# Performance work log

Hardware: AMD Instinct MI355X
Metric: run time of the kernel (lower is better)

Reference implementation:

```python
import jax, jax.numpy as jnp
import numpy as np

SMOOTHNESS_WEIGHT = 0.01
TRANSITION_PENALTY_WEIGHT = 0.1
NUM_CLASSES = 3

B, C, T = 512, 3, 16384


def setup_inputs() -> dict:
    key = jax.random.key(0)
    k1, k2 = jax.random.split(key)
    logits = jax.random.normal(k1, (B, C, T), dtype=jnp.float32)
    labels = jax.random.randint(k2, (B, T), 0, NUM_CLASSES, dtype=jnp.int64)
    return {"logits": logits, "labels": labels}


def reference(logits, labels):
    # --- cross entropy (mean over all B*T positions), logits [B, C, T] ---
    logp = jax.nn.log_softmax(logits, axis=1)                      # [B, C, T]
    nll = -jnp.take_along_axis(logp, labels[:, None, :], axis=1)   # [B, 1, T]
    ce = jnp.mean(nll)

    # --- smoothness: mean squared temporal difference of logits ---
    diff = jnp.mean((logits[:, :, 1:] - logits[:, :, :-1]) ** 2)
    smoothness_penalty = SMOOTHNESS_WEIGHT * diff

    # --- transition penalty: mean penalty over invalid (prev, next) pairs ---
    preds = jnp.argmax(logits, axis=1)                             # [B, T]
    # penalty lookup table: invalid transitions (0->2), (2->1), (1->0) = 1
    table = (jnp.zeros((NUM_CLASSES, NUM_CLASSES), dtype=jnp.float32)
             .at[0, 2].set(1.0).at[2, 1].set(1.0).at[1, 0].set(1.0))
    vals = table[preds[:, :-1], preds[:, 1:]]                      # [B, T-1]
    count = jnp.sum(vals > 0)
    # mean over invalid transitions only; 0.0 if none occur
    transition_penalty = TRANSITION_PENALTY_WEIGHT * jnp.where(
        count > 0, jnp.sum(vals) / jnp.maximum(count, 1).astype(vals.dtype), 0.0)

    return ce + smoothness_penalty + transition_penalty
```

## Files before the change

kernel.cpp:

```cpp
#include <hip/hip_runtime.h>

typedef float v4f __attribute__((ext_vector_type(4)));
typedef int   v4i __attribute__((ext_vector_type(4)));

#define BB 512
#define CC 3
#define TT 16384
#define NBLK 2048
#define NTHREADS (NBLK * 256)
#define NQUAD (BB * TT / 4)
#define ITERS (NQUAD / NTHREADS)

__global__ __launch_bounds__(256) void ce_trans_main(const float* __restrict__ logits,
                                                     const int* __restrict__ labels,
                                                     float* __restrict__ partials) {
    const int tid0 = blockIdx.x * 256 + threadIdx.x;
    const int lane = threadIdx.x & 63;

    float nll = 0.f, ss = 0.f;
    int cnt = 0;

    v4f A[2], Bv[2], Cv[2];
    v4i Lv[2];
    int TQ[2];
    const float* P0[2];

    auto issue = [&](int it, int slot) {
        const int q  = it * NTHREADS + tid0;
        const int b  = q >> 12;
        const int tq = q & 4095;
        const float* p0 = logits + (size_t)b * (CC * TT) + (tq << 2);
        A[slot]  = __builtin_nontemporal_load((const v4f*)p0);
        Bv[slot] = __builtin_nontemporal_load((const v4f*)(p0 + TT));
        Cv[slot] = __builtin_nontemporal_load((const v4f*)(p0 + 2 * TT));
        Lv[slot] = __builtin_nontemporal_load((const v4i*)(labels + (size_t)b * TT + (tq << 2)));
        TQ[slot] = tq;
        P0[slot] = p0;
    };

    auto compute = [&](int slot) {
        const v4f a = A[slot], bq = Bv[slot], c = Cv[slot];
        const v4i l = Lv[slot];
        const float x0[4] = {a.x,  a.y,  a.z,  a.w};
        const float x1[4] = {bq.x, bq.y, bq.z, bq.w};
        const float x2[4] = {c.x,  c.y,  c.z,  c.w};
        const int  lab[4] = {l.x,  l.y,  l.z,  l.w};
        int am[4];

#pragma unroll
        for (int j = 0; j < 4; ++j) {
            const float v0 = x0[j], v1 = x1[j], v2 = x2[j];
            int idx = 0;
            float mx = v0;
            if (v1 > mx) { mx = v1; idx = 1; }
            if (v2 > mx) { mx = v2; idx = 2; }
            am[j] = idx;
            const float e  = __expf(v0 - mx) + __expf(v1 - mx) + __expf(v2 - mx);
            const float xl = (lab[j] == 0) ? v0 : ((lab[j] == 1) ? v1 : v2);
            nll += mx + __logf(e) - xl;
        }

#pragma unroll
        for (int j = 0; j < 3; ++j) {
            const float d0 = x0[j + 1] - x0[j];
            const float d1 = x1[j + 1] - x1[j];
            const float d2 = x2[j + 1] - x2[j];
            ss += d0 * d0 + d1 * d1 + d2 * d2;
            cnt += (0x8C >> (3 * am[j] + am[j + 1])) & 1;
        }

        float xn0 = __shfl_down(x0[0], 1, 64);
        float xn1 = __shfl_down(x1[0], 1, 64);
        float xn2 = __shfl_down(x2[0], 1, 64);
        int   amn = __shfl_down(am[0], 1, 64);
        bool valid = true;
        if (lane == 63) {
            if (TQ[slot] == 4095) {
                valid = false;
            } else {
                const float* p0 = P0[slot];
                xn0 = p0[4]; xn1 = p0[TT + 4]; xn2 = p0[2 * TT + 4];
                int idx = 0;
                float mx = xn0;
                if (xn1 > mx) { mx = xn1; idx = 1; }
                if (xn2 > mx) { mx = xn2; idx = 2; }
                amn = idx;
            }
        }
        if (valid) {
            const float d0 = xn0 - x0[3];
            const float d1 = xn1 - x1[3];
            const float d2 = xn2 - x2[3];
            ss += d0 * d0 + d1 * d1 + d2 * d2;
            cnt += (0x8C >> (3 * am[3] + amn)) & 1;
        }
    };

    issue(0, 0);
#pragma unroll
    for (int it = 0; it < ITERS; ++it) {
        if (it + 1 < ITERS) issue(it + 1, (it + 1) & 1);
        compute(it & 1);
    }

    float fcnt = (float)cnt;
#pragma unroll
    for (int off = 32; off > 0; off >>= 1) {
        nll  += __shfl_down(nll,  off, 64);
        ss   += __shfl_down(ss,   off, 64);
        fcnt += __shfl_down(fcnt, off, 64);
    }

    __shared__ float s_nll[4], s_ss[4], s_cnt[4];
    const int wave = threadIdx.x >> 6;
    if ((threadIdx.x & 63) == 0) { s_nll[wave] = nll; s_ss[wave] = ss; s_cnt[wave] = fcnt; }
    __syncthreads();
    if (threadIdx.x == 0) {
        partials[blockIdx.x]            = s_nll[0] + s_nll[1] + s_nll[2] + s_nll[3];
        partials[NBLK + blockIdx.x]     = s_ss[0]  + s_ss[1]  + s_ss[2]  + s_ss[3];
        partials[2 * NBLK + blockIdx.x] = s_cnt[0] + s_cnt[1] + s_cnt[2] + s_cnt[3];
    }
}

__global__ __launch_bounds__(256) void ce_trans_final(const float* __restrict__ partials,
                                                      float* __restrict__ out) {
    float sn = 0.f, st = 0.f, sc = 0.f;
#pragma unroll
    for (int k = 0; k < 2; ++k) {
        const int i = k * 256 + threadIdx.x;
        const v4f n4 = *((const v4f*)partials + i);
        const v4f s4 = *((const v4f*)partials + 512 + i);
        const v4f c4 = *((const v4f*)partials + 1024 + i);
        sn += n4.x + n4.y + n4.z + n4.w;
        st += s4.x + s4.y + s4.z + s4.w;
        sc += c4.x + c4.y + c4.z + c4.w;
    }
#pragma unroll
    for (int off = 32; off > 0; off >>= 1) {
        sn += __shfl_down(sn, off, 64);
        st += __shfl_down(st, off, 64);
        sc += __shfl_down(sc, off, 64);
    }
    __shared__ float s_n[4], s_s[4], s_c[4];
    const int wave = threadIdx.x >> 6;
    if ((threadIdx.x & 63) == 0) { s_n[wave] = sn; s_s[wave] = st; s_c[wave] = sc; }
    __syncthreads();
    if (threadIdx.x == 0) {
        const float tn = s_n[0] + s_n[1] + s_n[2] + s_n[3];
        const float ts = s_s[0] + s_s[1] + s_s[2] + s_s[3];
        const float tc = s_c[0] + s_c[1] + s_c[2] + s_c[3];
        const float ce = tn / 8388608.0f;
        const float sm = 0.01f * (ts / 25164288.0f);
        const float tp = (tc > 0.5f) ? 0.1f : 0.0f;
        out[0] = ce + sm + tp;
    }
}

extern "C" void kernel_launch(void* const* d_in, const int* in_sizes, int n_in,
                              void* d_out, int out_size, void* d_ws, size_t ws_size,
                              hipStream_t stream) {
    const float* logits = (const float*)d_in[0];
    const int*   labels = (const int*)d_in[1];
    float* out      = (float*)d_out;
    float* partials = (float*)d_ws;

    ce_trans_main<<<NBLK, 256, 0, stream>>>(logits, labels, partials);
    ce_trans_final<<<1, 256, 0, stream>>>(partials, out);
}
```

Before: 166.2 us.

## Assign contiguous 16-element chunks per thread and issue all loads upfront

Each thread now processes a contiguous run of 16 timesteps of one batch row instead of four strided quads. All logits and label loads are issued at once, before compute, and the neighbour exchange via wave shuffles happens once per thread instead of once per quad. Launch bounds add an occupancy hint. This cuts shuffle and boundary overhead and raises memory-level parallelism, at the cost of more registers and less coalesced per-instruction access.

```diff
diff --git a/kernel.cpp b/kernel.cpp
--- a/kernel.cpp
+++ b/kernel.cpp
@@ -8,99 +8,91 @@
 #define TT 16384
 #define NBLK 2048
 #define NTHREADS (NBLK * 256)
-#define NQUAD (BB * TT / 4)
-#define ITERS (NQUAD / NTHREADS)
+#define CPR 1024
 
-__global__ __launch_bounds__(256) void ce_trans_main(const float* __restrict__ logits,
-                                                     const int* __restrict__ labels,
-                                                     float* __restrict__ partials) {
+__global__ __launch_bounds__(256, 4) void ce_trans_main(const float* __restrict__ logits,
+                                                        const int* __restrict__ labels,
+                                                        float* __restrict__ partials) {
     const int tid0 = blockIdx.x * 256 + threadIdx.x;
     const int lane = threadIdx.x & 63;
+    const int b    = tid0 >> 10;
+    const int cr   = tid0 & 1023;
+
+    const float* p0 = logits + (size_t)b * (CC * TT) + (cr << 4);
+    const int*   pl = labels + (size_t)b * TT + (cr << 4);
+
+    v4f A[4], Bv[4], Cv[4];
+    v4i Lv[4];
+#pragma unroll
+    for (int k = 0; k < 4; ++k) A[k]  = __builtin_nontemporal_load((const v4f*)p0 + k);
+#pragma unroll
+    for (int k = 0; k < 4; ++k) Bv[k] = __builtin_nontemporal_load((const v4f*)(p0 + TT) + k);
+#pragma unroll
+    for (int k = 0; k < 4; ++k) Cv[k] = __builtin_nontemporal_load((const v4f*)(p0 + 2 * TT) + k);
+#pragma unroll
+    for (int k = 0; k < 4; ++k) Lv[k] = __builtin_nontemporal_load((const v4i*)pl + k);
+
+    const bool tail = (lane == 63) && (cr != 1023);
+    float g0 = 0.f, g1 = 0.f, g2 = 0.f;
+    if (tail) {
+        g0 = __builtin_nontemporal_load(p0 + 16);
+        g1 = __builtin_nontemporal_load(p0 + TT + 16);
+        g2 = __builtin_nontemporal_load(p0 + 2 * TT + 16);
+    }
 
     float nll = 0.f, ss = 0.f;
     int cnt = 0;
 
-    v4f A[2], Bv[2], Cv[2];
-    v4i Lv[2];
-    int TQ[2];
-    const float* P0[2];
-
-    auto issue = [&](int it, int slot) {
-        const int q  = it * NTHREADS + tid0;
-        const int b  = q >> 12;
-        const int tq = q & 4095;
-        const float* p0 = logits + (size_t)b * (CC * TT) + (tq << 2);
-        A[slot]  = __builtin_nontemporal_load((const v4f*)p0);
-        Bv[slot] = __builtin_nontemporal_load((const v4f*)(p0 + TT));
-        Cv[slot] = __builtin_nontemporal_load((const v4f*)(p0 + 2 * TT));
-        Lv[slot] = __builtin_nontemporal_load((const v4i*)(labels + (size_t)b * TT + (tq << 2)));
-        TQ[slot] = tq;
-        P0[slot] = p0;
-    };
-
-    auto compute = [&](int slot) {
-        const v4f a = A[slot], bq = Bv[slot], c = Cv[slot];
-        const v4i l = Lv[slot];
-        const float x0[4] = {a.x,  a.y,  a.z,  a.w};
-        const float x1[4] = {bq.x, bq.y, bq.z, bq.w};
-        const float x2[4] = {c.x,  c.y,  c.z,  c.w};
-        const int  lab[4] = {l.x,  l.y,  l.z,  l.w};
-        int am[4];
+    float f00 = 0.f, f10 = 0.f, f20 = 0.f;
+    int   am0 = 0;
+    float pv0 = 0.f, pv1 = 0.f, pv2 = 0.f;
+    int   pam = 0;
 
 #pragma unroll
-        for (int j = 0; j < 4; ++j) {
-            const float v0 = x0[j], v1 = x1[j], v2 = x2[j];
-            int idx = 0;
-            float mx = v0;
-            if (v1 > mx) { mx = v1; idx = 1; }
-            if (v2 > mx) { mx = v2; idx = 2; }
-            am[j] = idx;
-            const float e  = __expf(v0 - mx) + __expf(v1 - mx) + __expf(v2 - mx);
-            const float xl = (lab[j] == 0) ? v0 : ((lab[j] == 1) ? v1 : v2);
-            nll += mx + __logf(e) - xl;
+    for (int t = 0; t < 16; ++t) {
+        const int k = t >> 2, j = t & 3;
+        const float v0 = A[k][j], v1 = Bv[k][j], v2 = Cv[k][j];
+        const int   lab = Lv[k][j];
+
+        int idx = 0;
+        float mx = v0;
+        if (v1 > mx) { mx = v1; idx = 1; }
+        if (v2 > mx) { mx = v2; idx = 2; }
+
+        const float e  = __expf(v0 - mx) + __expf(v1 - mx) + __expf(v2 - mx);
+        const float xl = (lab == 0) ? v0 : ((lab == 1) ? v1 : v2);
+        nll += mx + __logf(e) - xl;
+
+        if (t == 0) {
+            f00 = v0; f10 = v1; f20 = v2; am0 = idx;
+        } else {
+            const float d0 = v0 - pv0;
+            const float d1 = v1 - pv1;
+            const float d2 = v2 - pv2;
+            ss += d0 * d0 + d1 * d1 + d2 * d2;
+            cnt += (0x8C >> (3 * pam + idx)) & 1;
         }
+        pv0 = v0; pv1 = v1; pv2 = v2; pam = idx;
+    }
 
-#pragma unroll
-        for (int j = 0; j < 3; ++j) {
-            const float d0 = x0[j + 1] - x0[j];
-            const float d1 = x1[j + 1] - x1[j];
-            const float d2 = x2[j + 1] - x2[j];
-            ss += d0 * d0 + d1 * d1 + d2 * d2;
-            cnt += (0x8C >> (3 * am[j] + am[j + 1])) & 1;
-        }
-
-        float xn0 = __shfl_down(x0[0], 1, 64);
-        float xn1 = __shfl_down(x1[0], 1, 64);
-        float xn2 = __shfl_down(x2[0], 1, 64);
-        int   amn = __shfl_down(am[0], 1, 64);
-        bool valid = true;
-        if (lane == 63) {
-            if (TQ[slot] == 4095) {
-                valid = false;
-            } else {
-                const float* p0 = P0[slot];
-                xn0 = p0[4]; xn1 = p0[TT + 4]; xn2 = p0[2 * TT + 4];
-                int idx = 0;
-                float mx = xn0;
-                if (xn1 > mx) { mx = xn1; idx = 1; }
-                if (xn2 > mx) { mx = xn2; idx = 2; }
-                amn = idx;
-            }
-        }
-        if (valid) {
-            const float d0 = xn0 - x0[3];
-            const float d1 = xn1 - x1[3];
-            const float d2 = xn2 - x2[3];
-            ss += d0 * d0 + d1 * d1 + d2 * d2;
-            cnt += (0x8C >> (3 * am[3] + amn)) & 1;
-        }
-    };
-
-    issue(0, 0);
-#pragma unroll
-    for (int it = 0; it < ITERS; ++it) {
-        if (it + 1 < ITERS) issue(it + 1, (it + 1) & 1);
-        compute(it & 1);
+    float xn0 = __shfl_down(f00, 1, 64);
+    float xn1 = __shfl_down(f10, 1, 64);
+    float xn2 = __shfl_down(f20, 1, 64);
+    int   amn = __shfl_down(am0, 1, 64);
+    if (tail) {
+        xn0 = g0; xn1 = g1; xn2 = g2;
+        int idx = 0;
+        float mx = xn0;
+        if (xn1 > mx) { mx = xn1; idx = 1; }
+        if (xn2 > mx) { mx = xn2; idx = 2; }
+        amn = idx;
+    }
+    if (cr != 1023) {
+        const float d0 = xn0 - pv0;
+        const float d1 = xn1 - pv1;
+        const float d2 = xn2 - pv2;
+        ss += d0 * d0 + d1 * d1 + d2 * d2;
+        cnt += (0x8C >> (3 * pam + amn)) & 1;
     }
 
     float fcnt = (float)cnt;
```

New measurement: 175.1 us. +5.3%, slower.
